# Kernel optimization log

Hardware: AMD Instinct MI355X
Metric: run time of the kernel (lower is better)

Reference implementation:

```python
import jax, jax.numpy as jnp
import numpy as np

B, T, C = 8, 1024, 1024
H, HS = 16, 64            # n_head, head_size
K, STRIDE = 32, 16        # block_length, stride_length
WIN = 128                 # local_window_size
EPS = 1e-5


def _ln(z, w):
    m = jnp.mean(z, axis=-1, keepdims=True)
    v = jnp.var(z, axis=-1, keepdims=True)
    return (z - m) / jnp.sqrt(v + EPS) * w


def setup_inputs() -> dict:
    key = jax.random.key(0)
    ks = jax.random.split(key, 8)
    s = 0.02
    return {
        "x": jax.random.normal(ks[0], (B, T, C), jnp.float32),
        "c_attn_w": jax.random.normal(ks[1], (3 * C, C), jnp.float32) * s,
        "conv_w": jax.random.normal(ks[2], (HS, HS, K), jnp.float32) * s,
        "ln_comp_w": jnp.ones((HS,), jnp.float32),
        "ln_local_w": jnp.ones((C,), jnp.float32),
        "gate_w1": jax.random.normal(ks[3], (C, 2 * C), jnp.float32) * s,
        "gate_ln_w": jnp.ones((C,), jnp.float32),
        "gate_w2": jax.random.normal(ks[4], (2, C), jnp.float32) * s,
        "c_proj_w": jax.random.normal(ks[5], (C, C), jnp.float32) * s,
    }


def reference(x, c_attn_w, conv_w, ln_comp_w, ln_local_w, gate_w1, gate_ln_w, gate_w2, c_proj_w):
    qkv = jnp.einsum('btc,oc->bto', x, c_attn_w)          # [B,T,3C]
    q, k, v = jnp.split(qkv, 3, axis=-1)
    def heads(t):
        return t.reshape(B, T, H, HS).transpose(0, 2, 1, 3)  # [B,H,T,hs]
    q, k, v = heads(q), heads(k), heads(v)

    # CompressionMLP: Conv1d over time + LayerNorm(hs) + exact GELU
    def compress(t):
        xr = t.transpose(0, 1, 3, 2).reshape(B * H, HS, T)   # [B*H, hs, T]
        co = jax.lax.conv_general_dilated(
            xr, conv_w, window_strides=(STRIDE,), padding='VALID',
            dimension_numbers=('NCH', 'OIH', 'NCH'))          # [B*H, hs, NB]
        co = co.transpose(0, 2, 1)                            # [B*H, NB, hs]
        co = jax.nn.gelu(_ln(co, ln_comp_w), approximate=False)
        nb = co.shape[1]
        return co.reshape(B, H, nb, HS)

    kc = compress(k)
    vc = compress(v)
    NB = kc.shape[2]  # 63
    scale = 1.0 / np.sqrt(HS)

    ti = jnp.arange(T)
    band = (ti[None, :] <= ti[:, None]) & (ti[None, :] >= ti[:, None] - WIN)  # [T,T]
    s_loc = jnp.einsum('bhqd,bhkd->bhqk', q, k) * scale
    s_loc = jnp.where(band[None, None], s_loc, -jnp.inf)
    local_out = jnp.einsum('bhqk,bhkd->bhqd', jax.nn.softmax(s_loc, axis=-1), v)
    local_out = local_out.transpose(0, 2, 1, 3).reshape(B, T, C)
    local_norm = _ln(local_out, ln_local_w)

    # compressed-KV attention with block-causal mask: block j <= token i
    bj = jnp.arange(NB)
    cmask = bj[None, :] <= ti[:, None]                        # [T,NB]
    s_cmp = jnp.einsum('bhqd,bhkd->bhqk', q, kc) * scale
    s_cmp = jnp.where(cmask[None, None], s_cmp, -jnp.inf)
    comp_out = jnp.einsum('bhqk,bhkd->bhqd', jax.nn.softmax(s_cmp, axis=-1), vc)
    comp_out = comp_out.transpose(0, 2, 1, 3).reshape(B, T, C)

    # AttentionGating: last-token features -> Linear -> LN -> ReLU -> Linear -> softmax
    feats = jnp.concatenate([local_norm[:, -1, :], comp_out[:, -1, :]], axis=-1)  # [B,2C]
    h = jax.nn.relu(_ln(feats @ gate_w1.T, gate_ln_w))
    gates = jax.nn.softmax(h @ gate_w2.T, axis=-1)            # [B,2]

    combined = gates[:, None, 0:1] * local_norm + gates[:, None, 1:2] * comp_out
    y = jnp.einsum('btc,oc->bto', combined, c_proj_w)
    return y
```

## Files before the change

### kernel.cpp

```cpp
#include <hip/hip_runtime.h>
#include <cstdint>
#include <cmath>
#include <cstddef>

typedef unsigned int u32;
typedef unsigned short u16;
typedef __bf16 bf16x8 __attribute__((ext_vector_type(8)));
typedef float f32x4 __attribute__((ext_vector_type(4)));
typedef u32 u32x4 __attribute__((ext_vector_type(4)));
typedef u32 u32x2 __attribute__((ext_vector_type(2)));

#define DEV static __device__ __forceinline__

DEV float bflo(u32 u) { return __uint_as_float(u << 16); }
DEV float bfhi(u32 u) { return __uint_as_float(u & 0xffff0000u); }
DEV u16 f2bf(float f) {
  u32 u = __float_as_uint(f);
  u += 0x7fffu + ((u >> 16) & 1u);
  return (u16)(u >> 16);
}
DEV f32x4 unpack_bf4(u32x2 r) {
  return (f32x4){bflo(r[0]), bfhi(r[0]), bflo(r[1]), bfhi(r[1])};
}
DEV float wredsum(float v) {
#pragma unroll
  for (int o = 32; o; o >>= 1) v += __shfl_xor(v, o, 64);
  return v;
}

DEV void gload_lds16(const u16* g, u16* lds_base) {
  __builtin_amdgcn_global_load_lds((const __attribute__((address_space(1))) void*)g,
                                   (__attribute__((address_space(3))) void*)lds_base,
                                   16, 0, 0);
}

__global__ __launch_bounds__(256) void fused_cast(const float* __restrict__ x,
                                                  const float* __restrict__ aw,
                                                  const float* __restrict__ pw,
                                                  const float* __restrict__ cw,
                                                  u16* __restrict__ xb,
                                                  u16* __restrict__ wab,
                                                  u16* __restrict__ wpb,
                                                  u16* __restrict__ wcb,
                                                  u16* __restrict__ kcb,
                                                  u16* __restrict__ vcb) {
  const int blk = blockIdx.x;
  if (blk < 12288) {
    const float* src;
    u16* dst;
    int base;
    if (blk < 8192) { src = x; dst = xb; base = blk; }
    else if (blk < 11264) { src = aw; dst = wab; base = blk - 8192; }
    else { src = pw; dst = wpb; base = blk - 11264; }
    const size_t idx = ((size_t)base * 256 + threadIdx.x) * 4;
    const f32x4 v = *(const f32x4*)&src[idx];
    u32x2 r;
    r[0] = (u32)f2bf(v[0]) | ((u32)f2bf(v[1]) << 16);
    r[1] = (u32)f2bf(v[2]) | ((u32)f2bf(v[3]) << 16);
    *(u32x2*)&dst[idx] = r;
  } else if (blk < 12800) {
    const int idx = (blk - 12288) * 256 + threadIdx.x;
    const int o = idx >> 11;
    const int rest = idx & 2047;
    const int i = rest >> 5;
    const int kk = rest & 31;
    wcb[(o << 11) + (kk << 6) + i] = f2bf(cw[idx]);
  } else {
    for (int i = threadIdx.x; i < 8192; i += 256) {
      const int bh = i >> 6, d = i & 63;
      kcb[bh * 4096 + 63 * 64 + d] = 0;
      vcb[bh * 4096 + d * 64 + 63] = 0;
    }
  }
}

template <int OUT_BF16>
__global__ __launch_bounds__(256, 4) void gemm_bt(const u16* __restrict__ A,
                                                  const u16* __restrict__ Bm,
                                                  void* __restrict__ out,
                                                  int M, int N, int K) {
  __shared__ u16 As[128 * 64];
  __shared__ u16 Bs[128 * 64];
  const int tid = threadIdx.x;
  const int lane = tid & 63;
  const int w = tid >> 6;
  const int row0 = blockIdx.x * 128;
  const int col0 = blockIdx.y * 128;
  const int wm = (w >> 1) * 64, wn = (w & 1) * 64;
  const int lr = lane & 15, lq = lane >> 4;
  const int srow = lane >> 3;
  const int scol = ((lane & 7) ^ (srow & 7)) * 8;
  const int pgA = ((lq ^ (lr & 7)) * 8);

  f32x4 acc[4][4] = {};

  for (int k0 = 0; k0 < K; k0 += 64) {
    __syncthreads();
#pragma unroll
    for (int c = 0; c < 4; ++c) {
      const int base_r = w * 32 + c * 8;
      gload_lds16(&A[(size_t)(row0 + base_r + srow) * K + k0 + scol], &As[base_r * 64]);
      gload_lds16(&Bm[(size_t)(col0 + base_r + srow) * K + k0 + scol], &Bs[base_r * 64]);
    }
    __syncthreads();
#pragma unroll
    for (int ks = 0; ks < 2; ++ks) {
      const int pg = pgA ^ (ks << 5);
      bf16x8 af[4], bfr[4];
#pragma unroll
      for (int i = 0; i < 4; ++i) {
        af[i] = *(const bf16x8*)&As[(wm + i * 16 + lr) * 64 + pg];
        bfr[i] = *(const bf16x8*)&Bs[(wn + i * 16 + lr) * 64 + pg];
      }
#pragma unroll
      for (int i = 0; i < 4; ++i)
#pragma unroll
        for (int j = 0; j < 4; ++j)
          acc[i][j] = __builtin_amdgcn_mfma_f32_16x16x32_bf16(af[i], bfr[j], acc[i][j], 0, 0, 0);
    }
  }
#pragma unroll
  for (int i = 0; i < 4; ++i)
#pragma unroll
    for (int j = 0; j < 4; ++j)
#pragma unroll
      for (int rr = 0; rr < 4; ++rr) {
        const int gr = row0 + wm + i * 16 + lq * 4 + rr;
        const int gc = col0 + wn + j * 16 + lr;
        const float v = acc[i][j][rr];
        if (OUT_BF16)
          ((u16*)out)[(size_t)gr * N + gc] = f2bf(v);
        else
          ((float*)out)[(size_t)gr * N + gc] = v;
      }
}

__global__ __launch_bounds__(256) void compress_kernel(const u16* __restrict__ qkv,
                                                       const u16* __restrict__ Wc,
                                                       const float* __restrict__ ln_w,
                                                       u16* __restrict__ kcb,
                                                       u16* __restrict__ vcb) {
  __shared__ u16 As[2][32 * 32];
  __shared__ u16 Bs[2][64 * 32];
  __shared__ float Cs[32][65];
  const int tid = threadIdx.x;
  const int lane = tid & 63, w = tid >> 6;
  const int lr = lane & 15, lq = lane >> 4;
  const int r0 = blockIdx.x * 32;
  const int srcoff = 1024 + (int)blockIdx.y * 1024;

  const int srow = lane >> 2, scol = (lane & 3) * 8;
  const size_t bbase = (size_t)(w * 16 + srow) * 2048 + scol;
  size_t abase = 0;
  if (w < 2) {
    const int gr = r0 + w * 16 + srow;
    const int bh = gr / 63;
    const int nb = gr - bh * 63;
    const int b = bh >> 4, h = bh & 15;
    abase = (size_t)(b * 1024 + nb * 16) * 3072 + srcoff + h * 64 + scol;
  }
  const int rw = (w & 1) * 16;
  const int cw = (w >> 1) * 32;

  f32x4 acc[2] = {};
  gload_lds16(&Wc[bbase], &Bs[0][w * 512]);
  if (w < 2) gload_lds16(&qkv[abase], &As[0][w * 512]);
  for (int it = 0; it < 64; ++it) {
    const int cur = it & 1;
    __syncthreads();
    if (it < 63) {
      const int k0 = (it + 1) * 32;
      const int kk = k0 >> 6, i0 = k0 & 63;
      gload_lds16(&Wc[bbase + k0], &Bs[cur ^ 1][w * 512]);
      if (w < 2) gload_lds16(&qkv[abase + (size_t)kk * 3072 + i0], &As[cur ^ 1][w * 512]);
    }
    const bf16x8 af = *(const bf16x8*)&As[cur][(rw + lr) * 32 + lq * 8];
#pragma unroll
    for (int j = 0; j < 2; ++j) {
      const bf16x8 bfr = *(const bf16x8*)&Bs[cur][(cw + j * 16 + lr) * 32 + lq * 8];
      acc[j] = __builtin_amdgcn_mfma_f32_16x16x32_bf16(af, bfr, acc[j], 0, 0, 0);
    }
  }
  __syncthreads();
#pragma unroll
  for (int j = 0; j < 2; ++j)
#pragma unroll
    for (int rr = 0; rr < 4; ++rr)
      Cs[rw + lq * 4 + rr][cw + j * 16 + lr] = acc[j][rr];
  __syncthreads();
  if (tid < 32) {
    const int gr2 = r0 + tid;
    const int bh2 = gr2 / 63;
    const int nb2 = gr2 - bh2 * 63;
    float s = 0.f, s2 = 0.f;
#pragma unroll 8
    for (int d = 0; d < 64; ++d) {
      const float xv = Cs[tid][d];
      s += xv;
      s2 += xv * xv;
    }
    const float m = s * (1.f / 64.f);
    const float inv = rsqrtf(s2 * (1.f / 64.f) - m * m + 1e-5f);
    if (blockIdx.y == 0) {
      const size_t gb = (size_t)bh2 * 4096 + nb2 * 64;
#pragma unroll 8
      for (int d = 0; d < 64; ++d) {
        const float z = (Cs[tid][d] - m) * inv * ln_w[d];
        kcb[gb + d] = f2bf(0.5f * z * (1.f + erff(z * 0.70710678118f)));
      }
    } else {
      const size_t gb = (size_t)bh2 * 4096 + nb2;
#pragma unroll 8
      for (int d = 0; d < 64; ++d) {
        const float z = (Cs[tid][d] - m) * inv * ln_w[d];
        vcb[gb + d * 64] = f2bf(0.5f * z * (1.f + erff(z * 0.70710678118f)));
      }
    }
  }
}

__global__ __launch_bounds__(256) void attn_fused(const u16* __restrict__ qkv,
                                                  const u16* __restrict__ kcb,
                                                  const u16* __restrict__ vcb,
                                                  u16* __restrict__ loc,
                                                  u16* __restrict__ outc) {
  __shared__ __align__(16) char smem[53248];
  u16* Ks = (u16*)smem;
  u16* Vt = (u16*)smem;
  u16* Ps = (u16*)(smem + 27648);
  const int bh = blockIdx.x;
  const int b = bh >> 4, h = bh & 15;
  const int i0 = blockIdx.y * 64;
  const int jbase = i0 - 128;
  const int tid = threadIdx.x;
  const int lane = tid & 63, w = tid >> 6;
  const int lr = lane & 15, lq = lane >> 4;

  u32x4 vreg[6];
#pragma unroll
  for (int c = 0; c < 6; ++c) {
    const int lin = c * 256 + tid;
    const int s = lin >> 3, d0 = (lin & 7) * 8;
    const int j = jbase + s;
    u32x4 kval = {0, 0, 0, 0}, vval = {0, 0, 0, 0};
    if (j >= 0) {
      const size_t ro = (size_t)(b * 1024 + j) * 3072 + h * 64 + d0;
      kval = *(const u32x4*)&qkv[ro + 1024];
      vval = *(const u32x4*)&qkv[ro + 2048];
    }
    vreg[c] = vval;
    *(u32x4*)&Ks[s * 72 + d0] = kval;
  }
  bf16x8 qf[2];
  {
    const size_t qrow = (size_t)(b * 1024 + i0 + w * 16 + lr) * 3072 + h * 64;
#pragma unroll
    for (int ks = 0; ks < 2; ++ks) qf[ks] = *(const bf16x8*)&qkv[qrow + ks * 32 + lq * 8];
  }
  __syncthreads();

  f32x4 sa[9];
#pragma unroll
  for (int j9 = 0; j9 < 9; ++j9) sa[j9] = (f32x4){0.f, 0.f, 0.f, 0.f};
#pragma unroll
  for (int ks = 0; ks < 2; ++ks)
#pragma unroll
    for (int j9 = 0; j9 < 9; ++j9) {
      const int jt = w + j9;
      const bf16x8 kf = *(const bf16x8*)&Ks[(jt * 16 + lr) * 72 + ks * 32 + lq * 8];
      sa[j9] = __builtin_amdgcn_mfma_f32_16x16x32_bf16(qf[ks], kf, sa[j9], 0, 0, 0);
    }

  const float NINF = -__builtin_inff();
  float mx[4] = {NINF, NINF, NINF, NINF};
#pragma unroll
  for (int j9 = 0; j9 < 9; ++j9) {
    const int s = (w + j9) * 16 + lr;
#pragma unroll
    for (int rr = 0; rr < 4; ++rr) {
      const int qi = w * 16 + lq * 4 + rr;
      const bool valid = (jbase + s >= 0) && (s >= qi) && (s <= qi + 128);
      const float v = valid ? sa[j9][rr] * 0.125f : NINF;
      sa[j9][rr] = v;
      mx[rr] = fmaxf(mx[rr], v);
    }
  }
#pragma unroll
  for (int rr = 0; rr < 4; ++rr)
#pragma unroll
    for (int o = 1; o < 16; o <<= 1) mx[rr] = fmaxf(mx[rr], __shfl_xor(mx[rr], o, 64));
  float sum[4] = {0.f, 0.f, 0.f, 0.f};
#pragma unroll
  for (int j9 = 0; j9 < 9; ++j9)
#pragma unroll
    for (int rr = 0; rr < 4; ++rr) {
      const float p = __expf(sa[j9][rr] - mx[rr]);
      sa[j9][rr] = p;
      sum[rr] += p;
    }
#pragma unroll
  for (int rr = 0; rr < 4; ++rr) {
#pragma unroll
    for (int o = 1; o < 16; o <<= 1) sum[rr] += __shfl_xor(sum[rr], o, 64);
    sum[rr] = 1.0f / sum[rr];
  }
  __syncthreads();

#pragma unroll
  for (int j9 = 0; j9 < 9; ++j9) {
    const int jt = w + j9;
#pragma unroll
    for (int rr = 0; rr < 4; ++rr)
      Ps[(w * 16 + lq * 4 + rr) * 200 + jt * 16 + lr] = f2bf(sa[j9][rr] * sum[rr]);
  }
  {
    const int jz = (w == 0) ? 9 : (w == 1) ? 0 : (w == 2) ? 11 : 2;
#pragma unroll
    for (int rr = 0; rr < 4; ++rr) Ps[(w * 16 + lq * 4 + rr) * 200 + jz * 16 + lr] = 0;
  }
#pragma unroll
  for (int c = 0; c < 6; ++c) {
    const int lin = c * 256 + tid;
    const int s = lin >> 3, d0 = (lin & 7) * 8;
    const u32x4 val = vreg[c];
#pragma unroll
    for (int q = 0; q < 4; ++q) {
      Vt[(d0 + 2 * q) * 200 + s] = (u16)(val[q] & 0xffffu);
      Vt[(d0 + 2 * q + 1) * 200 + s] = (u16)(val[q] >> 16);
    }
  }
  __syncthreads();

  const int W = (w >> 1) * 32;
  f32x4 oa[4];
#pragma unroll
  for (int jt = 0; jt < 4; ++jt) oa[jt] = (f32x4){0.f, 0.f, 0.f, 0.f};
#pragma unroll
  for (int ks = 0; ks < 5; ++ks) {
    const bf16x8 pf = *(const bf16x8*)&Ps[(w * 16 + lr) * 200 + W + ks * 32 + lq * 8];
#pragma unroll
    for (int jt = 0; jt < 4; ++jt) {
      const bf16x8 vf = *(const bf16x8*)&Vt[(jt * 16 + lr) * 200 + W + ks * 32 + lq * 8];
      oa[jt] = __builtin_amdgcn_mfma_f32_16x16x32_bf16(pf, vf, oa[jt], 0, 0, 0);
    }
  }
#pragma unroll
  for (int jt = 0; jt < 4; ++jt)
#pragma unroll
    for (int rr = 0; rr < 4; ++rr)
      loc[(size_t)(b * 1024 + i0 + w * 16 + lq * 4 + rr) * 1024 + h * 64 + jt * 16 + lr] =
          f2bf(oa[jt][rr]);

  __syncthreads();
  u16* Kc = (u16*)smem;
  u16* Vc = (u16*)(smem + 9216);
  u16* Pc = (u16*)(smem + 18432);
  const size_t cb = (size_t)bh * 4096;
  for (int c2 = tid; c2 < 512; c2 += 256) {
    const int nb = c2 >> 3, d0 = (c2 & 7) * 8;
    *(u32x4*)&Kc[nb * 72 + d0] = *(const u32x4*)&kcb[cb + nb * 64 + d0];
  }
  for (int c2 = tid; c2 < 512; c2 += 256) {
    const int d = c2 >> 3, n0 = (c2 & 7) * 8;
    *(u32x4*)&Vc[d * 72 + n0] = *(const u32x4*)&vcb[cb + d * 64 + n0];
  }
  __syncthreads();

  f32x4 ca[4];
#pragma unroll
  for (int j = 0; j < 4; ++j) ca[j] = (f32x4){0.f, 0.f, 0.f, 0.f};
#pragma unroll
  for (int ks = 0; ks < 2; ++ks)
#pragma unroll
    for (int j = 0; j < 4; ++j) {
      const bf16x8 kf = *(const bf16x8*)&Kc[(j * 16 + lr) * 72 + ks * 32 + lq * 8];
      ca[j] = __builtin_amdgcn_mfma_f32_16x16x32_bf16(qf[ks], kf, ca[j], 0, 0, 0);
    }
  float mc[4] = {NINF, NINF, NINF, NINF};
#pragma unroll
  for (int j = 0; j < 4; ++j) {
    const int s = j * 16 + lr;
#pragma unroll
    for (int rr = 0; rr < 4; ++rr) {
      const int i = i0 + w * 16 + lq * 4 + rr;
      const bool valid = (s <= i) && (s < 63);
      const float v = valid ? ca[j][rr] * 0.125f : NINF;
      ca[j][rr] = v;
      mc[rr] = fmaxf(mc[rr], v);
    }
  }
#pragma unroll
  for (int rr = 0; rr < 4; ++rr)
#pragma unroll
    for (int o = 1; o < 16; o <<= 1) mc[rr] = fmaxf(mc[rr], __shfl_xor(mc[rr], o, 64));
  float sc[4] = {0.f, 0.f, 0.f, 0.f};
#pragma unroll
  for (int j = 0; j < 4; ++j)
#pragma unroll
    for (int rr = 0; rr < 4; ++rr) {
      const float p = __expf(ca[j][rr] - mc[rr]);
      ca[j][rr] = p;
      sc[rr] += p;
    }
#pragma unroll
  for (int rr = 0; rr < 4; ++rr) {
#pragma unroll
    for (int o = 1; o < 16; o <<= 1) sc[rr] += __shfl_xor(sc[rr], o, 64);
    sc[rr] = 1.0f / sc[rr];
  }
#pragma unroll
  for (int j = 0; j < 4; ++j)
#pragma unroll
    for (int rr = 0; rr < 4; ++rr)
      Pc[(w * 16 + lq * 4 + rr) * 72 + j * 16 + lr] = f2bf(ca[j][rr] * sc[rr]);
  __syncthreads();

  f32x4 co[4];
#pragma unroll
  for (int jt = 0; jt < 4; ++jt) co[jt] = (f32x4){0.f, 0.f, 0.f, 0.f};
#pragma unroll
  for (int ks = 0; ks < 2; ++ks) {
    const bf16x8 pf = *(const bf16x8*)&Pc[(w * 16 + lr) * 72 + ks * 32 + lq * 8];
#pragma unroll
    for (int jt = 0; jt < 4; ++jt) {
      const bf16x8 vf = *(const bf16x8*)&Vc[(jt * 16 + lr) * 72 + ks * 32 + lq * 8];
      co[jt] = __builtin_amdgcn_mfma_f32_16x16x32_bf16(pf, vf, co[jt], 0, 0, 0);
    }
  }
#pragma unroll
  for (int jt = 0; jt < 4; ++jt)
#pragma unroll
    for (int rr = 0; rr < 4; ++rr)
      outc[(size_t)(b * 1024 + i0 + w * 16 + lq * 4 + rr) * 1024 + h * 64 + jt * 16 + lr] =
          f2bf(co[jt][rr]);
}

__global__ __launch_bounds__(256) void ln_feats(const u16* __restrict__ locb,
                                                const u16* __restrict__ compb,
                                                const float* __restrict__ lnw,
                                                float* __restrict__ feats) {
  const int b = blockIdx.x, tid = threadIdx.x;
  const size_t base = ((size_t)b * 1024 + 1023) * 1024 + tid * 4;
  const f32x4 v = unpack_bf4(*(const u32x2*)&locb[base]);
  float s = v[0] + v[1] + v[2] + v[3];
  float s2 = v[0] * v[0] + v[1] * v[1] + v[2] * v[2] + v[3] * v[3];
  s = wredsum(s);
  s2 = wredsum(s2);
  __shared__ float rs[4], rs2[4];
  const int w = tid >> 6, lane = tid & 63;
  if (!lane) { rs[w] = s; rs2[w] = s2; }
  __syncthreads();
  s = rs[0] + rs[1] + rs[2] + rs[3];
  s2 = rs2[0] + rs2[1] + rs2[2] + rs2[3];
  const float m = s * (1.f / 1024.f);
  const float inv = rsqrtf(s2 * (1.f / 1024.f) - m * m + 1e-5f);
  const f32x4 wv = *(const f32x4*)&lnw[tid * 4];
  f32x4 o;
#pragma unroll
  for (int k = 0; k < 4; ++k) o[k] = (v[k] - m) * inv * wv[k];
  *(f32x4*)&feats[b * 2048 + tid * 4] = o;
  *(f32x4*)&feats[b * 2048 + 1024 + tid * 4] = unpack_bf4(*(const u32x2*)&compb[base]);
}

__global__ __launch_bounds__(256) void gate_gemv(const float* __restrict__ feats,
                                                 const float* __restrict__ w1,
                                                 float* __restrict__ hraw) {
  const int o = blockIdx.x * 4 + (threadIdx.x >> 6);
  const int lane = threadIdx.x & 63;
  const float* wr = &w1[(size_t)o * 2048];
  float acc[8] = {};
#pragma unroll
  for (int it = 0; it < 8; ++it) {
    const int c = (it * 64 + lane) * 4;
    const f32x4 wv = *(const f32x4*)&wr[c];
#pragma unroll
    for (int b = 0; b < 8; ++b) {
      const f32x4 fv = *(const f32x4*)&feats[b * 2048 + c];
      acc[b] += fv[0] * wv[0] + fv[1] * wv[1] + fv[2] * wv[2] + fv[3] * wv[3];
    }
  }
#pragma unroll
  for (int b = 0; b < 8; ++b) acc[b] = wredsum(acc[b]);
  if (lane == 0) {
#pragma unroll
    for (int b = 0; b < 8; ++b) hraw[b * 1024 + o] = acc[b];
  }
}

__global__ __launch_bounds__(256) void gate_fin(const float* __restrict__ hraw,
                                                const float* __restrict__ lnw,
                                                const float* __restrict__ w2,
                                                float* __restrict__ gates) {
  const int b = blockIdx.x, tid = threadIdx.x;
  const f32x4 v = *(const f32x4*)&hraw[(size_t)b * 1024 + tid * 4];
  float s = v[0] + v[1] + v[2] + v[3];
  float s2 = v[0] * v[0] + v[1] * v[1] + v[2] * v[2] + v[3] * v[3];
  s = wredsum(s);
  s2 = wredsum(s2);
  __shared__ float rs[4], rs2[4];
  const int w = tid >> 6, lane = tid & 63;
  if (!lane) { rs[w] = s; rs2[w] = s2; }
  __syncthreads();
  s = rs[0] + rs[1] + rs[2] + rs[3];
  s2 = rs2[0] + rs2[1] + rs2[2] + rs2[3];
  const float m = s * (1.f / 1024.f);
  const float inv = rsqrtf(s2 * (1.f / 1024.f) - m * m + 1e-5f);
  float p0 = 0.f, p1 = 0.f;
#pragma unroll
  for (int k = 0; k < 4; ++k) {
    float hh = (v[k] - m) * inv * lnw[tid * 4 + k];
    hh = fmaxf(hh, 0.f);
    p0 += hh * w2[tid * 4 + k];
    p1 += hh * w2[1024 + tid * 4 + k];
  }
  p0 = wredsum(p0);
  p1 = wredsum(p1);
  __syncthreads();
  if (!lane) { rs[w] = p0; rs2[w] = p1; }
  __syncthreads();
  if (tid == 0) {
    const float l0 = rs[0] + rs[1] + rs[2] + rs[3];
    const float l1 = rs2[0] + rs2[1] + rs2[2] + rs2[3];
    const float mm = fmaxf(l0, l1);
    const float e0 = __expf(l0 - mm), e1 = __expf(l1 - mm);
    const float iv = 1.f / (e0 + e1);
    gates[b * 2] = e0 * iv;
    gates[b * 2 + 1] = e1 * iv;
  }
}

__global__ __launch_bounds__(256) void combine_ln_cast(const u16* __restrict__ locb,
                                                       const u16* __restrict__ compb,
                                                       const float* __restrict__ lnw,
                                                       const float* __restrict__ gates,
                                                       u16* __restrict__ outb) {
  const int row = blockIdx.x, tid = threadIdx.x;
  const size_t base = (size_t)row * 1024 + tid * 4;
  const f32x4 v = unpack_bf4(*(const u32x2*)&locb[base]);
  float s = v[0] + v[1] + v[2] + v[3];
  float s2 = v[0] * v[0] + v[1] * v[1] + v[2] * v[2] + v[3] * v[3];
  s = wredsum(s);
  s2 = wredsum(s2);
  __shared__ float rs[4], rs2[4];
  const int w = tid >> 6, lane = tid & 63;
  if (!lane) { rs[w] = s; rs2[w] = s2; }
  __syncthreads();
  s = rs[0] + rs[1] + rs[2] + rs[3];
  s2 = rs2[0] + rs2[1] + rs2[2] + rs2[3];
  const float m = s * (1.f / 1024.f);
  const float inv = rsqrtf(s2 * (1.f / 1024.f) - m * m + 1e-5f);
  const int b = row >> 10;
  const float g0 = gates[2 * b], g1 = gates[2 * b + 1];
  const f32x4 wv = *(const f32x4*)&lnw[tid * 4];
  const f32x4 c = unpack_bf4(*(const u32x2*)&compb[base]);
  float ov[4];
#pragma unroll
  for (int k = 0; k < 4; ++k) ov[k] = g0 * ((v[k] - m) * inv * wv[k]) + g1 * c[k];
  u32x2 r;
  r[0] = (u32)f2bf(ov[0]) | ((u32)f2bf(ov[1]) << 16);
  r[1] = (u32)f2bf(ov[2]) | ((u32)f2bf(ov[3]) << 16);
  *(u32x2*)&outb[base] = r;
}

extern "C" void kernel_launch(void* const* d_in, const int* in_sizes, int n_in,
                              void* d_out, int out_size, void* d_ws, size_t ws_size,
                              hipStream_t stream) {
  const float* x = (const float*)d_in[0];
  const float* c_attn_w = (const float*)d_in[1];
  const float* conv_w = (const float*)d_in[2];
  const float* ln_comp_w = (const float*)d_in[3];
  const float* ln_local_w = (const float*)d_in[4];
  const float* gate_w1 = (const float*)d_in[5];
  const float* gate_ln_w = (const float*)d_in[6];
  const float* gate_w2 = (const float*)d_in[7];
  const float* c_proj_w = (const float*)d_in[8];
  float* y = (float*)d_out;

  char* ws = (char*)d_ws;
  size_t off = 0;
  auto alloc = [&](size_t bytes) -> void* {
    void* p = ws + off;
    off += (bytes + 255) & ~(size_t)255;
    return p;
  };
  u16* qkvb = (u16*)alloc((size_t)8192 * 3072 * 2);
  u16* xb = (u16*)alloc((size_t)8192 * 1024 * 2);
  u16* wab = (u16*)alloc((size_t)3072 * 1024 * 2);
  u16* wpb = (u16*)alloc((size_t)1024 * 1024 * 2);
  u16* wcb = (u16*)alloc((size_t)64 * 2048 * 2);
  u16* kcb = (u16*)alloc((size_t)128 * 4096 * 2);
  u16* vcb = (u16*)alloc((size_t)128 * 4096 * 2);
  u16* locb = (u16*)alloc((size_t)8192 * 1024 * 2);
  u16* compb = (u16*)alloc((size_t)8192 * 1024 * 2);
  float* feats = (float*)alloc((size_t)8 * 2048 * 4);
  float* hraw = (float*)alloc((size_t)8192 * 4);
  float* gates = (float*)alloc(64);
  u16* combb = (u16*)alloc((size_t)8192 * 1024 * 2);

  fused_cast<<<12801, 256, 0, stream>>>(x, c_attn_w, c_proj_w, conv_w, xb, wab, wpb, wcb, kcb,
                                        vcb);

  gemm_bt<1><<<dim3(64, 24), 256, 0, stream>>>(xb, wab, qkvb, 8192, 3072, 1024);

  compress_kernel<<<dim3(252, 2), 256, 0, stream>>>(qkvb, wcb, ln_comp_w, kcb, vcb);

  attn_fused<<<dim3(128, 16), 256, 0, stream>>>(qkvb, kcb, vcb, locb, compb);

  ln_feats<<<8, 256, 0, stream>>>(locb, compb, ln_local_w, feats);
  gate_gemv<<<256, 256, 0, stream>>>(feats, gate_w1, hraw);
  gate_fin<<<8, 256, 0, stream>>>(hraw, gate_ln_w, gate_w2, gates);

  combine_ln_cast<<<8192, 256, 0, stream>>>(locb, compb, ln_local_w, gates, combb);

  gemm_bt<0><<<dim3(64, 8), 256, 0, stream>>>(combb, wpb, y, 8192, 1024, 1024);
}
```

Before: 292.9 us.

## Replace QKV projection GEMM with 256x256-tile 8-wave pipelined kernel

```diff
diff --git a/kernel.cpp b/kernel.cpp
--- a/kernel.cpp
+++ b/kernel.cpp
@@ -135,6 +135,106 @@
       }
 }
 
+#define GATE4 asm volatile("s_waitcnt vmcnt(4)" ::: "memory")
+#define GATE0 asm volatile("s_waitcnt vmcnt(0)" ::: "memory")
+
+#define G8_PHASE(TT, R, C, STAGES, GATE)                                           \
+  do {                                                                             \
+    const int buf_ = ((TT) & 1) << 14;                                             \
+    bf16x8 af_[2][4], bf_[2][2];                                                   \
+    _Pragma("unroll") for (int ks = 0; ks < 2; ++ks) {                             \
+      const int pg_ = pgA ^ (ks << 5);                                             \
+      _Pragma("unroll") for (int m = 0; m < 4; ++m)                                \
+          af_[ks][m] =                                                             \
+              *(const bf16x8*)&As[buf_ + (wm + (R) * 64 + m * 16 + lr) * 64 + pg_];\
+      _Pragma("unroll") for (int n = 0; n < 2; ++n)                                \
+          bf_[ks][n] =                                                             \
+              *(const bf16x8*)&Bs[buf_ + (wn + (C) * 32 + n * 16 + lr) * 64 + pg_];\
+    }                                                                              \
+    STAGES                                                                         \
+    __builtin_amdgcn_s_barrier();                                                  \
+    __builtin_amdgcn_s_setprio(1);                                                 \
+    _Pragma("unroll") for (int ks = 0; ks < 2; ++ks)                               \
+        _Pragma("unroll") for (int m = 0; m < 4; ++m)                              \
+            _Pragma("unroll") for (int n = 0; n < 2; ++n)                          \
+                acc[(R) * 4 + m][(C) * 2 + n] =                                    \
+                    __builtin_amdgcn_mfma_f32_16x16x32_bf16(                       \
+                        af_[ks][m], bf_[ks][n], acc[(R) * 4 + m][(C) * 2 + n],     \
+                        0, 0, 0);                                                  \
+    __builtin_amdgcn_s_setprio(0);                                                 \
+    GATE                                                                           \
+    __builtin_amdgcn_s_barrier();                                                  \
+  } while (0)
+
+__global__ __launch_bounds__(512, 2) void gemm8(const u16* __restrict__ A,
+                                                const u16* __restrict__ Bm,
+                                                u16* __restrict__ out,
+                                                int M, int N, int K) {
+  extern __shared__ __align__(16) u16 sm8[];
+  u16* As = sm8;
+  u16* Bs = sm8 + 32768;
+  const int tid = threadIdx.x;
+  const int lane = tid & 63;
+  const int w = tid >> 6;
+  const int row0 = blockIdx.x * 256;
+  const int col0 = blockIdx.y * 256;
+  const int wm = (w >> 2) * 128;
+  const int wn = (w & 3) * 64;
+  const int lr = lane & 15, lq = lane >> 4;
+  const int sgl = lane >> 3;
+  const int scol = ((lane & 7) ^ sgl) * 8;
+  const int pgA = (lq ^ (lr & 7)) * 8;
+  const int NKT = K >> 6;
+  const int NI = NKT >> 1;
+
+  auto stA = [&](int t, int r, int j) {
+    const int rb = j * 128 + r * 64 + w * 8;
+    gload_lds16(&A[(size_t)(row0 + rb + sgl) * K + (t << 6) + scol],
+                &As[((t & 1) << 14) + rb * 64]);
+  };
+  auto stB = [&](int t, int c, int j) {
+    const int rb = j * 128 + (w >> 2) * 64 + c * 32 + (w & 3) * 8;
+    gload_lds16(&Bm[(size_t)(col0 + rb + sgl) * K + (t << 6) + scol],
+                &Bs[((t & 1) << 14) + rb * 64]);
+  };
+
+  f32x4 acc[8][4] = {};
+
+  stA(0, 0, 0); stA(0, 0, 1); stA(0, 1, 0); stA(0, 1, 1);
+  stB(0, 0, 0); stB(0, 0, 1); stB(0, 1, 0); stB(0, 1, 1);
+  stB(1, 0, 0); stB(1, 0, 1); stA(1, 1, 0); stA(1, 1, 1);
+  GATE4;
+  __builtin_amdgcn_s_barrier();
+
+#pragma unroll 1
+  for (int i = 0; i < NI; ++i) {
+    const int t0 = 2 * i, t1 = t0 + 1;
+    const bool more = (i + 1 < NI);
+    G8_PHASE(t0, 0, 0, { stA(t1, 0, 0); stA(t1, 0, 1); }, ;);
+    G8_PHASE(t0, 1, 0, { stB(t1, 1, 0); stB(t1, 1, 1); }, ;);
+    G8_PHASE(t0, 1, 1, { if (more) { stB(t0 + 2, 0, 0); stB(t0 + 2, 0, 1); } }, ;);
+    G8_PHASE(t0, 0, 1, { if (more) { stA(t0 + 2, 1, 0); stA(t0 + 2, 1, 1); } },
+             { if (more) { GATE4; } else { GATE0; } });
+    G8_PHASE(t1, 0, 0, { if (more) { stA(t0 + 2, 0, 0); stA(t0 + 2, 0, 1); } }, ;);
+    G8_PHASE(t1, 1, 0, { if (more) { stB(t0 + 2, 1, 0); stB(t0 + 2, 1, 1); } }, ;);
+    G8_PHASE(t1, 1, 1, { if (more) { stB(t0 + 3, 0, 0); stB(t0 + 3, 0, 1); } }, ;);
+    G8_PHASE(t1, 0, 1, { if (more) { stA(t0 + 3, 1, 0); stA(t0 + 3, 1, 1); } },
+             { GATE4; });
+  }
+  GATE0;
+
+#pragma unroll
+  for (int mt = 0; mt < 8; ++mt)
+#pragma unroll
+    for (int nt = 0; nt < 4; ++nt)
+#pragma unroll
+      for (int rr = 0; rr < 4; ++rr) {
+        const int gr = row0 + wm + mt * 16 + lq * 4 + rr;
+        const int gc = col0 + wn + nt * 16 + lr;
+        out[(size_t)gr * N + gc] = f2bf(acc[mt][nt][rr]);
+      }
+}
+
 __global__ __launch_bounds__(256) void compress_kernel(const u16* __restrict__ qkv,
                                                        const u16* __restrict__ Wc,
                                                        const float* __restrict__ ln_w,
@@ -575,6 +675,13 @@
   const float* gate_w2 = (const float*)d_in[7];
   const float* c_proj_w = (const float*)d_in[8];
   float* y = (float*)d_out;
+
+  static bool attr_done = false;
+  if (!attr_done) {
+    hipFuncSetAttribute(reinterpret_cast<const void*>(gemm8),
+                        hipFuncAttributeMaxDynamicSharedMemorySize, 131072);
+    attr_done = true;
+  }
 
   char* ws = (char*)d_ws;
   size_t off = 0;
@@ -600,7 +707,7 @@
   fused_cast<<<12801, 256, 0, stream>>>(x, c_attn_w, c_proj_w, conv_w, xb, wab, wpb, wcb, kcb,
                                         vcb);
 
-  gemm_bt<1><<<dim3(64, 24), 256, 0, stream>>>(xb, wab, qkvb, 8192, 3072, 1024);
+  gemm8<<<dim3(32, 12), 512, 131072, stream>>>(xb, wab, qkvb, 8192, 3072, 1024);
 
   compress_kernel<<<dim3(252, 2), 256, 0, stream>>>(qkvb, wcb, ln_comp_w, kcb, vcb);
 
```

Measured after the change: 297.5 us. About the same (+1.6%).
